# Kernel tuning notes

Measured on AMD Instinct MI355X. Metric: run time of the kernel, lower is better.

Reference implementation:

```python
import jax, jax.numpy as jnp
import numpy as np

N = 20000   # nodes
R = 8       # base out-degree (ring circulant), plus self-loop
K = 3       # hops: supports of A, A^2, A^3
IN_DIM = 128
HID = 64


def _edges(m):
    # support of A^m for circulant ring with self-loops: dst i receives from (i-t) mod N, t=0..m*R
    deg = m * R + 1
    dst = np.repeat(np.arange(N, dtype=np.int32), deg)
    src = (dst - np.tile(np.arange(deg, dtype=np.int32), N)) % N
    return jnp.asarray(src), jnp.asarray(dst)


def setup_inputs() -> dict:
    key = jax.random.key(0)
    ks = jax.random.split(key, 8)
    def xavier(k, shape):
        fan_out, fan_in = shape[0], shape[1]
        std = np.float32(np.sqrt(2.0) * np.sqrt(2.0 / (fan_in + fan_out)))  # gain('relu')
        return jax.random.normal(k, shape, jnp.float32) * std
    inp = {
        "h": jax.random.normal(ks[0], (N, IN_DIM), jnp.float32),
        "fc_enc": xavier(ks[1], (HID, IN_DIM)),
        "diff_enc": xavier(ks[2], (HID, IN_DIM)),
        "att_enc": xavier(ks[3], (HID, 1)),
        "fc_dec": xavier(ks[4], (IN_DIM, HID)),
        "diff_dec": xavier(ks[5], (IN_DIM, HID)),
        "att_dec": xavier(ks[6], (IN_DIM, 1)),
        "att_comb": xavier(ks[7], (HID, 1)),
    }
    for m in range(1, K + 1):
        s, d = _edges(m)
        inp[f"src{m}"] = s
        inp[f"dst{m}"] = d
    return inp


def _gdn_layer(src, dst, h, Wfc, Wdiff, att, use_elu):
    z = h @ Wfc.T                      # [N, out]
    hd = h @ Wdiff.T                   # [N, out]
    d = hd[src] - hd[dst]              # edge gather-diff [E, out]
    e = jax.nn.leaky_relu(d @ att)     # [E, 1], torch default slope 0.01
    # edge softmax over incoming edges of each dst node
    emax = jax.ops.segment_max(e, dst, num_segments=N)
    ex = jnp.exp(e - emax[dst])
    den = jax.ops.segment_sum(ex, dst, num_segments=N)
    a = ex / den[dst]                  # [E, 1]
    agg = jax.ops.segment_sum(a * d, dst, num_segments=N)  # scatter-sum
    out = z + agg
    return jax.nn.elu(out) if use_elu else out


def reference(h, fc_enc, diff_enc, att_enc, fc_dec, diff_dec, att_dec, att_comb,
              src1, dst1, src2, dst2, src3, dst3):
    hops = [(src1, dst1), (src2, dst2), (src3, dst3)]
    Zs = [_gdn_layer(s, d, h, fc_enc, diff_enc, att_enc, True) for s, d in hops]
    e = jnp.concatenate([Z @ att_comb for Z in Zs], axis=-1)   # [N, K]
    a = jax.nn.softmax(jax.nn.leaky_relu(e), axis=-1)          # [N, K]
    z = jnp.einsum('nk,nhk->nh', a, jnp.stack(Zs, axis=-1))    # hop-attention combine
    # decoder runs on the last hop's graph (A^K), as in the torch code
    x = _gdn_layer(src3, dst3, z, fc_dec, diff_dec, att_dec, False)
    return x
```

## Files before the change

### kernel.cpp

```cpp
#include <hip/hip_runtime.h>
#include <math.h>

#define NN 20000

typedef __attribute__((ext_vector_type(8))) short short8;
typedef __attribute__((ext_vector_type(4))) float floatx4;

__device__ __forceinline__ int wrapN(int r) {
    if (r < 0) r += NN;
    if (r >= NN) r -= NN;
    return r;
}
__device__ __forceinline__ unsigned f2bf(float f) {
    unsigned int u = __float_as_uint(f);
    u = (u + 0x7FFFu + ((u >> 16) & 1u)) >> 16;
    return u;
}

__global__ __launch_bounds__(256) void k0_prep(
    const float* __restrict__ fce, const float* __restrict__ dfe,
    const float* __restrict__ atte, const float* __restrict__ fcd,
    const float* __restrict__ dfd, const float* __restrict__ attd,
    unsigned short* __restrict__ Wenc, unsigned short* __restrict__ Wdec,
    float* __restrict__ uenc, float* __restrict__ vdec)
{
    const int idx = blockIdx.x * 256 + threadIdx.x;
    {
        int r = idx >> 7, k = idx & 127;
        float v = (r < 64) ? fce[r * 128 + k] : dfe[(r - 64) * 128 + k];
        Wenc[r * 128 + k] = (unsigned short)f2bf(v);
    }
    {
        int r = idx >> 6, k = idx & 63;
        float v = (r < 128) ? fcd[r * 64 + k] : dfd[(r - 128) * 64 + k];
        Wdec[r * 64 + k] = (unsigned short)f2bf(v);
    }
    if (blockIdx.x == 0 && threadIdx.x < 128) {
        int k = threadIdx.x; float s = 0.f;
        for (int j = 0; j < 64; j++) s = fmaf(atte[j], dfe[j * 128 + k], s);
        uenc[k] = s;
    }
    if (blockIdx.x == 1 && threadIdx.x < 64) {
        int k = threadIdx.x; float s = 0.f;
        for (int c = 0; c < 128; c++) s = fmaf(attd[c], dfd[c * 64 + k], s);
        vdec[k] = s;
    }
}

__global__ __launch_bounds__(256) void kA_enc(
    const float* __restrict__ h, const unsigned short* __restrict__ Wenc,
    const float* __restrict__ uenc, const float* __restrict__ attc,
    const float* __restrict__ vdec, unsigned short* __restrict__ zcb,
    float* __restrict__ gd)
{
    __shared__ __align__(16) float smem[3856];
    unsigned short* Hs = (unsigned short*)smem;
    float* hdw = smem;
    float* zw  = smem + 2720;
    float* gw  = smem + 3808;

    const int tid  = threadIdx.x;
    const int n0   = blockIdx.x * 16;
    const int lane = tid & 63;
    const int wv   = tid >> 6;
    const int m16  = lane & 15;
    const int quad = lane >> 4;

    for (int idx = tid; idx < 768; idx += 256) {
        int r = idx >> 4, c = (idx & 15) << 3;
        const float* hp = h + wrapN(n0 - 24 + r) * 128 + c;
        float4 a = *(const float4*)hp;
        float4 b = *(const float4*)(hp + 4);
        uint4 pk;
        pk.x = f2bf(a.x) | (f2bf(a.y) << 16);
        pk.y = f2bf(a.z) | (f2bf(a.w) << 16);
        pk.z = f2bf(b.x) | (f2bf(b.y) << 16);
        pk.w = f2bf(b.z) | (f2bf(b.w) << 16);
        *(uint4*)(Hs + r * 136 + c) = pk;
        float4 ua = *(const float4*)(uenc + c);
        float4 ub = *(const float4*)(uenc + c + 4);
        float p = a.x * ua.x + a.y * ua.y + a.z * ua.z + a.w * ua.w
                + b.x * ub.x + b.y * ub.y + b.z * ub.z + b.w * ub.w;
#pragma unroll
        for (int off = 1; off <= 8; off <<= 1) p += __shfl_xor(p, off, 64);
        if ((idx & 15) == 0) gw[r] = p;
    }
    __syncthreads();

    floatx4 acc[3][2];
#pragma unroll
    for (int a = 0; a < 3; a++)
#pragma unroll
        for (int b = 0; b < 2; b++) acc[a][b] = (floatx4){0.f, 0.f, 0.f, 0.f};

#pragma unroll
    for (int ks = 0; ks < 4; ks++) {
        const int kk = ks * 32 + quad * 8;
        const int jr0 = 32 * wv + m16;
        short8 B0 = *(const short8*)(Wenc + jr0 * 128 + kk);
        short8 B1 = *(const short8*)(Wenc + (jr0 + 16) * 128 + kk);
        short8 A[3];
#pragma unroll
        for (int mt = 0; mt < 3; mt++)
            A[mt] = *(short8*)(Hs + (mt * 16 + m16) * 136 + kk);
#pragma unroll
        for (int mt = 0; mt < 3; mt++) {
            acc[mt][0] = __builtin_amdgcn_mfma_f32_16x16x32_bf16(A[mt], B0, acc[mt][0], 0, 0, 0);
            acc[mt][1] = __builtin_amdgcn_mfma_f32_16x16x32_bf16(A[mt], B1, acc[mt][1], 0, 0, 0);
        }
    }
    __syncthreads();

#pragma unroll
    for (int mt = 0; mt < 3; mt++)
#pragma unroll
        for (int nt2 = 0; nt2 < 2; nt2++)
#pragma unroll
            for (int r = 0; r < 4; r++) {
                const int row = mt * 16 + quad * 4 + r;
                const int col = 32 * wv + nt2 * 16 + m16;
                const float val = acc[mt][nt2][r];
                if (col >= 64) { if (row < 40) hdw[row * 68 + (col - 64)] = val; }
                else if (row >= 24 && row < 40) zw[(row - 24) * 68 + col] = val;
            }
    __syncthreads();

    const int wvid = tid >> 6;
    const int half = (tid >> 5) & 1;
    const int l    = tid & 31;
    const float2 ac = *(const float2*)(attc + 2 * l);
    const float2 vd = *(const float2*)(vdec + 2 * l);

    for (int it = 0; it < 2; it++) {
        const int li   = 8 * it + 2 * wvid + half;
        const int node = n0 + li;
        const int loc  = 24 + li;

        const float g0 = gw[loc];
        const int t = l;
        float d = 0.f;
        if (t >= 1 && t < 25) {
            d = gw[loc - t] - g0;
            d = d > 0.f ? d : 0.01f * d;
        }
        float dm = (t < 25) ? d : -1e30f;
#pragma unroll
        for (int off = 16; off; off >>= 1) dm = fmaxf(dm, __shfl_xor(dm, off, 64));
        const float e = (t < 25) ? __expf(d - dm) : 0.f;
        float s1 = (t < 9) ? e : 0.f, s2 = (t < 17) ? e : 0.f, s3 = e;
#pragma unroll
        for (int off = 16; off; off >>= 1) {
            s1 += __shfl_xor(s1, off, 64);
            s2 += __shfl_xor(s2, off, 64);
            s3 += __shfl_xor(s3, off, 64);
        }
        const float rd0 = 1.f / s1, rd1 = 1.f / s2, rd2 = 1.f / s3;

        const float2 zi = *(const float2*)(zw + li * 68 + 2 * l);
        const float2 h0 = *(const float2*)(hdw + loc * 68 + 2 * l);

        float2 s = {0.f, 0.f};
        float2 Z[3]; float eh[3];
#pragma unroll
        for (int m = 0; m < 3; m++) {
            const int lo = (m == 0) ? 0 : (m == 1 ? 9 : 17);
            const int hi = (m == 0) ? 9 : (m == 1 ? 17 : 25);
#pragma unroll
            for (int t2 = lo; t2 < hi; t2++) {
                const float et = __shfl(e, (half << 5) + t2, 64);
                const float2 hv = *(const float2*)(hdw + (loc - t2) * 68 + 2 * l);
                s.x = fmaf(et, hv.x, s.x);
                s.y = fmaf(et, hv.y, s.y);
            }
            const float rden = (m == 0) ? rd0 : (m == 1 ? rd1 : rd2);
            float ox = zi.x + s.x * rden - h0.x;
            float oy = zi.y + s.y * rden - h0.y;
            Z[m].x = ox > 0.f ? ox : __expf(ox) - 1.f;
            Z[m].y = oy > 0.f ? oy : __expf(oy) - 1.f;
            float p = Z[m].x * ac.x + Z[m].y * ac.y;
#pragma unroll
            for (int off = 16; off; off >>= 1) p += __shfl_xor(p, off, 64);
            eh[m] = p;
        }
#pragma unroll
        for (int m = 0; m < 3; m++) eh[m] = eh[m] > 0.f ? eh[m] : 0.01f * eh[m];
        const float mx = fmaxf(eh[0], fmaxf(eh[1], eh[2]));
        const float w0 = __expf(eh[0] - mx), w1 = __expf(eh[1] - mx), w2 = __expf(eh[2] - mx);
        const float wd = 1.f / (w0 + w1 + w2);
        float2 o;
        o.x = (w0 * Z[0].x + w1 * Z[1].x + w2 * Z[2].x) * wd;
        o.y = (w0 * Z[0].y + w1 * Z[1].y + w2 * Z[2].y) * wd;
        *(unsigned int*)(zcb + node * 64 + 2 * l) =
            f2bf(o.x) | (f2bf(o.y) << 16);
        float q = o.x * vd.x + o.y * vd.y;
#pragma unroll
        for (int off = 16; off; off >>= 1) q += __shfl_xor(q, off, 64);
        if (l == 0) gd[node] = q;
    }
}

__global__ __launch_bounds__(256) void kB_dec(
    const unsigned short* __restrict__ zcb, const unsigned short* __restrict__ Wdec,
    const float* __restrict__ gd, float* __restrict__ out)
{
    __shared__ __align__(16) float smem[7928];
    unsigned short* Zs  = (unsigned short*)smem;
    unsigned short* hdB = (unsigned short*)smem;
    float* zdw = smem + 2304;
    float* h0w = smem + 4480;
    unsigned short* Eb = (unsigned short*)(smem + 6656);
    float* gw  = smem + 7808;
    float* dmw = smem + 7864;
    float* rdw = smem + 7896;

    const int tid  = threadIdx.x;
    const int tile = blockIdx.x >> 1;
    const int ch   = blockIdx.x & 1;
    const int n0   = tile * 32;
    const int lane = tid & 63;
    const int wv   = tid >> 6;
    const int m16  = lane & 15;
    const int quad = lane >> 4;

    if (tid < 56) gw[tid] = gd[wrapN(n0 - 24 + tid)];

    for (int idx = tid; idx < 512; idx += 256) {
        int r = idx >> 3, c = (idx & 7) << 3;
        *(short8*)(Zs + r * 72 + c) =
            *(const short8*)(zcb + wrapN(n0 - 24 + r) * 64 + c);
    }
    __syncthreads();

    floatx4 acc[4][2];
#pragma unroll
    for (int a = 0; a < 4; a++)
#pragma unroll
        for (int b = 0; b < 2; b++) acc[a][b] = (floatx4){0.f, 0.f, 0.f, 0.f};

#pragma unroll
    for (int ks = 0; ks < 2; ks++) {
        const int kk = ks * 32 + quad * 8;
        const int c0 = 32 * wv + m16;
        const int wr0 = (c0 < 64) ? (ch * 64 + c0) : (128 + ch * 64 + (c0 - 64));
        const int c1 = c0 + 16;
        const int wr1 = (c1 < 64) ? (ch * 64 + c1) : (128 + ch * 64 + (c1 - 64));
        short8 B0 = *(const short8*)(Wdec + wr0 * 64 + kk);
        short8 B1 = *(const short8*)(Wdec + wr1 * 64 + kk);
        short8 A[4];
#pragma unroll
        for (int mt = 0; mt < 4; mt++)
            A[mt] = *(short8*)(Zs + (mt * 16 + m16) * 72 + kk);
#pragma unroll
        for (int mt = 0; mt < 4; mt++) {
            acc[mt][0] = __builtin_amdgcn_mfma_f32_16x16x32_bf16(A[mt], B0, acc[mt][0], 0, 0, 0);
            acc[mt][1] = __builtin_amdgcn_mfma_f32_16x16x32_bf16(A[mt], B1, acc[mt][1], 0, 0, 0);
        }
    }
    __syncthreads();

#pragma unroll
    for (int mt = 0; mt < 4; mt++)
#pragma unroll
        for (int nt2 = 0; nt2 < 2; nt2++) {
            const int colL = 32 * wv + nt2 * 16 + m16;
            const int rowB = mt * 16 + quad * 4;
            if (colL >= 64) {
                const int f = colL - 64;
                if (rowB < 56) {
                    uint2 pk;
                    pk.x = f2bf(acc[mt][nt2][0]) | (f2bf(acc[mt][nt2][1]) << 16);
                    pk.y = f2bf(acc[mt][nt2][2]) | (f2bf(acc[mt][nt2][3]) << 16);
                    *(uint2*)(hdB + f * 72 + rowB) = pk;
                }
#pragma unroll
                for (int r = 0; r < 4; r++) {
                    const int row = rowB + r;
                    if (row >= 24 && row < 56) h0w[(row - 24) * 68 + f] = acc[mt][nt2][r];
                }
            } else {
#pragma unroll
                for (int r = 0; r < 4; r++) {
                    const int row = rowB + r;
                    if (row >= 24 && row < 56) zdw[(row - 24) * 68 + colL] = acc[mt][nt2][r];
                }
            }
        }
    for (int idx = tid; idx < 512; idx += 256) {
        int f = idx >> 3, kk = 56 + ((idx & 7) << 1);
        *(unsigned*)(hdB + f * 72 + kk) = 0;
    }

    {
        const int half = (tid >> 5) & 1;
        const int l    = tid & 31;
        for (int it = 0; it < 4; it++) {
            const int li  = 8 * it + 2 * wv + half;
            const int loc = 24 + li;
            const float g0 = gw[loc];
            const int t = l;
            float d = 0.f;
            if (t >= 1 && t < 25) {
                d = gw[loc - t] - g0;
                d = d > 0.f ? d : 0.01f * d;
            }
            float dm = (t < 25) ? d : -1e30f;
#pragma unroll
            for (int off = 16; off; off >>= 1) dm = fmaxf(dm, __shfl_xor(dm, off, 64));
            const float e = (t < 25) ? __expf(d - dm) : 0.f;
            float s3 = e;
#pragma unroll
            for (int off = 16; off; off >>= 1) s3 += __shfl_xor(s3, off, 64);
            if (l == 0) { dmw[li] = dm; rdw[li] = 1.f / s3; }
        }
    }
    __syncthreads();

    for (int idx = tid; idx < 1152; idx += 256) {
        const int n  = idx / 36;
        const int kk = (idx - n * 36) * 2;
        const float g0 = gw[n + 24];
        const float em = dmw[n], rd = rdw[n];
        unsigned pk = 0;
#pragma unroll
        for (int j = 0; j < 2; j++) {
            const int k = kk + j;
            const bool in = (k >= n) && (k <= n + 24);
            const int kc = in ? k : 0;
            float d = gw[kc] - g0;
            d = d > 0.f ? d : 0.01f * d;
            const float e = in ? __expf(d - em) * rd : 0.f;
            pk |= f2bf(e) << (16 * j);
        }
        *(unsigned*)(Eb + n * 72 + kk) = pk;
    }
    __syncthreads();

    floatx4 wacc[2];
    wacc[0] = (floatx4){0.f, 0.f, 0.f, 0.f};
    wacc[1] = (floatx4){0.f, 0.f, 0.f, 0.f};
#pragma unroll
    for (int ks = 0; ks < 2; ks++) {
        const int kk = ks * 32 + quad * 8;
        short8 Bf = *(short8*)(hdB + (wv * 16 + m16) * 72 + kk);
        short8 A0 = *(short8*)(Eb + m16 * 72 + kk);
        short8 A1 = *(short8*)(Eb + (16 + m16) * 72 + kk);
        wacc[0] = __builtin_amdgcn_mfma_f32_16x16x32_bf16(A0, Bf, wacc[0], 0, 0, 0);
        wacc[1] = __builtin_amdgcn_mfma_f32_16x16x32_bf16(A1, Bf, wacc[1], 0, 0, 0);
    }

#pragma unroll
    for (int mt2 = 0; mt2 < 2; mt2++)
#pragma unroll
        for (int r = 0; r < 4; r++) {
            const int n = mt2 * 16 + quad * 4 + r;
            const int f = wv * 16 + m16;
            const float o = zdw[n * 68 + f] + wacc[mt2][r] - h0w[n * 68 + f];
            out[(n0 + n) * 128 + ch * 64 + f] = o;
        }
}

extern "C" void kernel_launch(void* const* d_in, const int* in_sizes, int n_in,
                              void* d_out, int out_size, void* d_ws, size_t ws_size,
                              hipStream_t stream)
{
    const float* h        = (const float*)d_in[0];
    const float* fc_enc   = (const float*)d_in[1];
    const float* diff_enc = (const float*)d_in[2];
    const float* att_enc  = (const float*)d_in[3];
    const float* fc_dec   = (const float*)d_in[4];
    const float* diff_dec = (const float*)d_in[5];
    const float* att_dec  = (const float*)d_in[6];
    const float* att_comb = (const float*)d_in[7];

    float* out = (float*)d_out;
    float* ws  = (float*)d_ws;
    float*          uenc = ws;
    float*          vdec = ws + 128;
    float*          gd   = ws + 192;
    unsigned short* zcb  = (unsigned short*)(ws + 192 + NN);
    unsigned short* Wenc = zcb + NN * 64;
    unsigned short* Wdec = Wenc + 128 * 128;
    (void)ws_size; (void)in_sizes; (void)n_in; (void)out_size;

    hipLaunchKernelGGL(k0_prep, dim3(64), dim3(256), 0, stream,
                       fc_enc, diff_enc, att_enc, fc_dec, diff_dec, att_dec,
                       Wenc, Wdec, uenc, vdec);
    hipLaunchKernelGGL(kA_enc, dim3(NN / 16), dim3(256), 0, stream,
                       h, Wenc, uenc, att_comb, vdec, zcb, gd);
    hipLaunchKernelGGL(kB_dec, dim3(2 * (NN / 32)), dim3(256), 0, stream,
                       zcb, Wdec, gd, out);
}
```

Measured before the change: 121.6 us.

## Move encoder edge aggregation onto MFMA with banded softmax weight matrices

The encoder kernel now processes 32 nodes per block instead of 16, which reduces the redundant 24-row halo GEMM work per node. The per-node scalar shuffle-and-FMA aggregation over neighbor diffs is replaced by MFMA products. These multiply a bf16 hi/lo split of the hd tile against banded bf16 exp-weight matrices, one per hop, with the softmax normalisation done separately. The hop-attention reduction moves to shared memory across waves. This adds much more LDS use (about 52KB), extra syncs and bf16 rounding of the weights, in exchange for replacing many LDS loads and shuffles with matrix instructions.

```diff
diff --git a/kernel.cpp b/kernel.cpp
--- a/kernel.cpp
+++ b/kernel.cpp
@@ -15,6 +15,9 @@
     unsigned int u = __float_as_uint(f);
     u = (u + 0x7FFFu + ((u >> 16) & 1u)) >> 16;
     return u;
+}
+__device__ __forceinline__ float bfval(float f) {
+    return __uint_as_float(f2bf(f) << 16);
 }
 
 __global__ __launch_bounds__(256) void k0_prep(
@@ -47,26 +50,35 @@
     }
 }
 
-__global__ __launch_bounds__(256) void kA_enc(
+__global__ __launch_bounds__(256, 2) void kA_enc(
     const float* __restrict__ h, const unsigned short* __restrict__ Wenc,
     const float* __restrict__ uenc, const float* __restrict__ attc,
     const float* __restrict__ vdec, unsigned short* __restrict__ zcb,
     float* __restrict__ gd)
 {
-    __shared__ __align__(16) float smem[3856];
+    __shared__ __align__(16) float smem[13088];
+    float* zw  = smem;
+    float* h0w = smem + 2176;
+    unsigned short* hdB = (unsigned short*)(smem + 4352);
+    unsigned short* hdL = (unsigned short*)(smem + 6656);
+    unsigned short* Eb  = (unsigned short*)(smem + 8960);
+    float* gw  = smem + 12416;
+    float* dmw = smem + 12480;
+    float* rdw = smem + 12512;
+    float* ehp = smem + 12608;
+    float* ehw = smem + 12992;
     unsigned short* Hs = (unsigned short*)smem;
-    float* hdw = smem;
-    float* zw  = smem + 2720;
-    float* gw  = smem + 3808;
 
     const int tid  = threadIdx.x;
-    const int n0   = blockIdx.x * 16;
+    const int n0   = blockIdx.x * 32;
     const int lane = tid & 63;
     const int wv   = tid >> 6;
     const int m16  = lane & 15;
     const int quad = lane >> 4;
 
-    for (int idx = tid; idx < 768; idx += 256) {
+    for (int idx = tid; idx < 3456; idx += 256) ((unsigned*)Eb)[idx] = 0u;
+
+    for (int idx = tid; idx < 1024; idx += 256) {
         int r = idx >> 4, c = (idx & 15) << 3;
         const float* hp = h + wrapN(n0 - 24 + r) * 128 + c;
         float4 a = *(const float4*)hp;
@@ -87,9 +99,43 @@
     }
     __syncthreads();
 
-    floatx4 acc[3][2];
-#pragma unroll
-    for (int a = 0; a < 3; a++)
+    {
+        const int half = (tid >> 5) & 1;
+        const int l    = tid & 31;
+#pragma unroll
+        for (int it = 0; it < 4; it++) {
+            const int li  = 8 * it + 2 * wv + half;
+            const int loc = 24 + li;
+            const float g0 = gw[loc];
+            float d = 0.f;
+            if (l >= 1 && l < 25) {
+                d = gw[loc - l] - g0;
+                d = d > 0.f ? d : 0.01f * d;
+            }
+            float dm = (l < 25) ? d : -1e30f;
+#pragma unroll
+            for (int off = 16; off; off >>= 1) dm = fmaxf(dm, __shfl_xor(dm, off, 64));
+            const float e  = (l < 25) ? __expf(d - dm) : 0.f;
+            const float er = bfval(e);
+            float s1 = (l < 9) ? er : 0.f, s2 = (l < 17) ? er : 0.f, s3 = er;
+#pragma unroll
+            for (int off = 16; off; off >>= 1) {
+                s1 += __shfl_xor(s1, off, 64);
+                s2 += __shfl_xor(s2, off, 64);
+                s3 += __shfl_xor(s3, off, 64);
+            }
+            if (l == 0) {
+                dmw[li] = dm;
+                rdw[li]      = 1.f / s1;
+                rdw[32 + li] = 1.f / s2;
+                rdw[64 + li] = 1.f / s3;
+            }
+        }
+    }
+
+    floatx4 acc[4][2];
+#pragma unroll
+    for (int a = 0; a < 4; a++)
 #pragma unroll
         for (int b = 0; b < 2; b++) acc[a][b] = (floatx4){0.f, 0.f, 0.f, 0.f};
 
@@ -99,12 +145,12 @@
         const int jr0 = 32 * wv + m16;
         short8 B0 = *(const short8*)(Wenc + jr0 * 128 + kk);
         short8 B1 = *(const short8*)(Wenc + (jr0 + 16) * 128 + kk);
-        short8 A[3];
-#pragma unroll
-        for (int mt = 0; mt < 3; mt++)
+        short8 A[4];
+#pragma unroll
+        for (int mt = 0; mt < 4; mt++)
             A[mt] = *(short8*)(Hs + (mt * 16 + m16) * 136 + kk);
 #pragma unroll
-        for (int mt = 0; mt < 3; mt++) {
+        for (int mt = 0; mt < 4; mt++) {
             acc[mt][0] = __builtin_amdgcn_mfma_f32_16x16x32_bf16(A[mt], B0, acc[mt][0], 0, 0, 0);
             acc[mt][1] = __builtin_amdgcn_mfma_f32_16x16x32_bf16(A[mt], B1, acc[mt][1], 0, 0, 0);
         }
@@ -112,90 +158,158 @@
     __syncthreads();
 
 #pragma unroll
-    for (int mt = 0; mt < 3; mt++)
-#pragma unroll
-        for (int nt2 = 0; nt2 < 2; nt2++)
+    for (int mt = 0; mt < 4; mt++)
+#pragma unroll
+        for (int nt2 = 0; nt2 < 2; nt2++) {
+            const int colL = 32 * wv + nt2 * 16 + m16;
+            const int rowB = mt * 16 + quad * 4;
+            if (colL >= 64) {
+                const int f = colL - 64;
+                if (rowB < 56) {
+                    const unsigned b0 = f2bf(acc[mt][nt2][0]);
+                    const unsigned b1 = f2bf(acc[mt][nt2][1]);
+                    const unsigned b2 = f2bf(acc[mt][nt2][2]);
+                    const unsigned b3 = f2bf(acc[mt][nt2][3]);
+                    uint2 pk;
+                    pk.x = b0 | (b1 << 16);
+                    pk.y = b2 | (b3 << 16);
+                    *(uint2*)(hdB + f * 72 + rowB) = pk;
+                    uint2 pl;
+                    pl.x =  f2bf(acc[mt][nt2][0] - __uint_as_float(b0 << 16))
+                         | (f2bf(acc[mt][nt2][1] - __uint_as_float(b1 << 16)) << 16);
+                    pl.y =  f2bf(acc[mt][nt2][2] - __uint_as_float(b2 << 16))
+                         | (f2bf(acc[mt][nt2][3] - __uint_as_float(b3 << 16)) << 16);
+                    *(uint2*)(hdL + f * 72 + rowB) = pl;
+                }
+#pragma unroll
+                for (int r = 0; r < 4; r++) {
+                    const int row = rowB + r;
+                    if (row >= 24 && row < 56) h0w[(row - 24) * 68 + f] = acc[mt][nt2][r];
+                }
+            } else {
+#pragma unroll
+                for (int r = 0; r < 4; r++) {
+                    const int row = rowB + r;
+                    if (row >= 24 && row < 56) zw[(row - 24) * 68 + colL] = acc[mt][nt2][r];
+                }
+            }
+        }
+    for (int idx = tid; idx < 1024; idx += 256) {
+        const int j = idx & 511;
+        const int f = j >> 3, kk = 56 + ((j & 7) << 1);
+        unsigned short* p = (idx >> 9) ? hdL : hdB;
+        *(unsigned*)(p + f * 72 + kk) = 0u;
+    }
+
+    for (int idx = tid; idx < 800; idx += 256) {
+        const int n = idx / 25, t = idx - n * 25;
+        const int loc = n + 24;
+        float d = 0.f;
+        if (t >= 1) {
+            d = gw[loc - t] - gw[loc];
+            d = d > 0.f ? d : 0.01f * d;
+        }
+        const float e = __expf(d - dmw[n]);
+        const int m = (t < 9) ? 0 : ((t < 17) ? 1 : 2);
+        Eb[m * 2304 + n * 72 + (loc - t)] = (unsigned short)f2bf(e);
+    }
+    __syncthreads();
+
+    const int fbase = wv * 16 + quad * 4;
+    const float4 ac4 = *(const float4*)(attc + fbase);
+    short8 Af0 = *(short8*)(hdB + (wv * 16 + m16) * 72 + quad * 8);
+    short8 Af1 = *(short8*)(hdB + (wv * 16 + m16) * 72 + 32 + quad * 8);
+    short8 Al0 = *(short8*)(hdL + (wv * 16 + m16) * 72 + quad * 8);
+    short8 Al1 = *(short8*)(hdL + (wv * 16 + m16) * 72 + 32 + quad * 8);
+
+    floatx4 wacc[2];
+    wacc[0] = (floatx4){0.f, 0.f, 0.f, 0.f};
+    wacc[1] = (floatx4){0.f, 0.f, 0.f, 0.f};
+    float Zr[3][2][4];
+    float pm[3][2];
+#pragma unroll
+    for (int m = 0; m < 3; m++) { pm[m][0] = 0.f; pm[m][1] = 0.f; }
+
+#pragma unroll
+    for (int m = 0; m < 3; m++) {
+        const unsigned short* Em = Eb + m * 2304;
+        short8 E00 = *(const short8*)(Em + m16 * 72 + quad * 8);
+        short8 E01 = *(const short8*)(Em + m16 * 72 + 32 + quad * 8);
+        short8 E10 = *(const short8*)(Em + (16 + m16) * 72 + quad * 8);
+        short8 E11 = *(const short8*)(Em + (16 + m16) * 72 + 32 + quad * 8);
+        wacc[0] = __builtin_amdgcn_mfma_f32_16x16x32_bf16(Af0, E00, wacc[0], 0, 0, 0);
+        wacc[0] = __builtin_amdgcn_mfma_f32_16x16x32_bf16(Al0, E00, wacc[0], 0, 0, 0);
+        wacc[0] = __builtin_amdgcn_mfma_f32_16x16x32_bf16(Af1, E01, wacc[0], 0, 0, 0);
+        wacc[0] = __builtin_amdgcn_mfma_f32_16x16x32_bf16(Al1, E01, wacc[0], 0, 0, 0);
+        wacc[1] = __builtin_amdgcn_mfma_f32_16x16x32_bf16(Af0, E10, wacc[1], 0, 0, 0);
+        wacc[1] = __builtin_amdgcn_mfma_f32_16x16x32_bf16(Al0, E10, wacc[1], 0, 0, 0);
+        wacc[1] = __builtin_amdgcn_mfma_f32_16x16x32_bf16(Af1, E11, wacc[1], 0, 0, 0);
+        wacc[1] = __builtin_amdgcn_mfma_f32_16x16x32_bf16(Al1, E11, wacc[1], 0, 0, 0);
+#pragma unroll
+        for (int nt = 0; nt < 2; nt++) {
+            const int n = nt * 16 + m16;
+            const float rd = rdw[m * 32 + n];
+            const float4 zv = *(const float4*)(zw + n * 68 + fbase);
+            const float4 hv = *(const float4*)(h0w + n * 68 + fbase);
 #pragma unroll
             for (int r = 0; r < 4; r++) {
-                const int row = mt * 16 + quad * 4 + r;
-                const int col = 32 * wv + nt2 * 16 + m16;
-                const float val = acc[mt][nt2][r];
-                if (col >= 64) { if (row < 40) hdw[row * 68 + (col - 64)] = val; }
-                else if (row >= 24 && row < 40) zw[(row - 24) * 68 + col] = val;
-            }
-    __syncthreads();
-
-    const int wvid = tid >> 6;
-    const int half = (tid >> 5) & 1;
-    const int l    = tid & 31;
-    const float2 ac = *(const float2*)(attc + 2 * l);
-    const float2 vd = *(const float2*)(vdec + 2 * l);
-
-    for (int it = 0; it < 2; it++) {
-        const int li   = 8 * it + 2 * wvid + half;
-        const int node = n0 + li;
-        const int loc  = 24 + li;
-
-        const float g0 = gw[loc];
-        const int t = l;
-        float d = 0.f;
-        if (t >= 1 && t < 25) {
-            d = gw[loc - t] - g0;
-            d = d > 0.f ? d : 0.01f * d;
-        }
-        float dm = (t < 25) ? d : -1e30f;
-#pragma unroll
-        for (int off = 16; off; off >>= 1) dm = fmaxf(dm, __shfl_xor(dm, off, 64));
-        const float e = (t < 25) ? __expf(d - dm) : 0.f;
-        float s1 = (t < 9) ? e : 0.f, s2 = (t < 17) ? e : 0.f, s3 = e;
-#pragma unroll
-        for (int off = 16; off; off >>= 1) {
-            s1 += __shfl_xor(s1, off, 64);
-            s2 += __shfl_xor(s2, off, 64);
-            s3 += __shfl_xor(s3, off, 64);
-        }
-        const float rd0 = 1.f / s1, rd1 = 1.f / s2, rd2 = 1.f / s3;
-
-        const float2 zi = *(const float2*)(zw + li * 68 + 2 * l);
-        const float2 h0 = *(const float2*)(hdw + loc * 68 + 2 * l);
-
-        float2 s = {0.f, 0.f};
-        float2 Z[3]; float eh[3];
-#pragma unroll
-        for (int m = 0; m < 3; m++) {
-            const int lo = (m == 0) ? 0 : (m == 1 ? 9 : 17);
-            const int hi = (m == 0) ? 9 : (m == 1 ? 17 : 25);
-#pragma unroll
-            for (int t2 = lo; t2 < hi; t2++) {
-                const float et = __shfl(e, (half << 5) + t2, 64);
-                const float2 hv = *(const float2*)(hdw + (loc - t2) * 68 + 2 * l);
-                s.x = fmaf(et, hv.x, s.x);
-                s.y = fmaf(et, hv.y, s.y);
-            }
-            const float rden = (m == 0) ? rd0 : (m == 1 ? rd1 : rd2);
-            float ox = zi.x + s.x * rden - h0.x;
-            float oy = zi.y + s.y * rden - h0.y;
-            Z[m].x = ox > 0.f ? ox : __expf(ox) - 1.f;
-            Z[m].y = oy > 0.f ? oy : __expf(oy) - 1.f;
-            float p = Z[m].x * ac.x + Z[m].y * ac.y;
-#pragma unroll
-            for (int off = 16; off; off >>= 1) p += __shfl_xor(p, off, 64);
-            eh[m] = p;
-        }
-#pragma unroll
-        for (int m = 0; m < 3; m++) eh[m] = eh[m] > 0.f ? eh[m] : 0.01f * eh[m];
-        const float mx = fmaxf(eh[0], fmaxf(eh[1], eh[2]));
-        const float w0 = __expf(eh[0] - mx), w1 = __expf(eh[1] - mx), w2 = __expf(eh[2] - mx);
+                const float val = ((const float*)&zv)[r] + wacc[nt][r] * rd
+                                - ((const float*)&hv)[r];
+                const float z = val > 0.f ? val : __expf(val) - 1.f;
+                Zr[m][nt][r] = z;
+                pm[m][nt] = fmaf(z, ((const float*)&ac4)[r], pm[m][nt]);
+            }
+        }
+    }
+
+#pragma unroll
+    for (int m = 0; m < 3; m++)
+#pragma unroll
+        for (int nt = 0; nt < 2; nt++) {
+            float p = pm[m][nt];
+            p += __shfl_xor(p, 16, 64);
+            p += __shfl_xor(p, 32, 64);
+            pm[m][nt] = p;
+        }
+    if (quad == 0) {
+#pragma unroll
+        for (int nt = 0; nt < 2; nt++)
+#pragma unroll
+            for (int m = 0; m < 3; m++)
+                ehp[wv * 96 + (nt * 16 + m16) * 3 + m] = pm[m][nt];
+    }
+    __syncthreads();
+    if (tid < 96) {
+        const float s = ehp[tid] + ehp[96 + tid] + ehp[192 + tid] + ehp[288 + tid];
+        ehw[tid] = s > 0.f ? s : 0.01f * s;
+    }
+    __syncthreads();
+
+#pragma unroll
+    for (int nt = 0; nt < 2; nt++) {
+        const int n = nt * 16 + m16;
+        const float e0 = ehw[n * 3], e1 = ehw[n * 3 + 1], e2 = ehw[n * 3 + 2];
+        const float mx = fmaxf(e0, fmaxf(e1, e2));
+        const float w0 = __expf(e0 - mx), w1 = __expf(e1 - mx), w2 = __expf(e2 - mx);
         const float wd = 1.f / (w0 + w1 + w2);
-        float2 o;
-        o.x = (w0 * Z[0].x + w1 * Z[1].x + w2 * Z[2].x) * wd;
-        o.y = (w0 * Z[0].y + w1 * Z[1].y + w2 * Z[2].y) * wd;
-        *(unsigned int*)(zcb + node * 64 + 2 * l) =
-            f2bf(o.x) | (f2bf(o.y) << 16);
+        float4 o;
+        o.x = (w0 * Zr[0][nt][0] + w1 * Zr[1][nt][0] + w2 * Zr[2][nt][0]) * wd;
+        o.y = (w0 * Zr[0][nt][1] + w1 * Zr[1][nt][1] + w2 * Zr[2][nt][1]) * wd;
+        o.z = (w0 * Zr[0][nt][2] + w1 * Zr[1][nt][2] + w2 * Zr[2][nt][2]) * wd;
+        o.w = (w0 * Zr[0][nt][3] + w1 * Zr[1][nt][3] + w2 * Zr[2][nt][3]) * wd;
+        *(float4*)(zw + n * 68 + fbase) = o;
+    }
+    __syncthreads();
+
+    for (int idx = tid; idx < 1024; idx += 256) {
+        const int ln = idx >> 5, l = idx & 31;
+        const float2 o = *(const float2*)(zw + ln * 68 + 2 * l);
+        *(unsigned*)(zcb + (n0 + ln) * 64 + 2 * l) = f2bf(o.x) | (f2bf(o.y) << 16);
+        const float2 vd = *(const float2*)(vdec + 2 * l);
         float q = o.x * vd.x + o.y * vd.y;
 #pragma unroll
         for (int off = 16; off; off >>= 1) q += __shfl_xor(q, off, 64);
-        if (l == 0) gd[node] = q;
+        if (l == 0) gd[n0 + ln] = q;
     }
 }
 
@@ -385,7 +499,7 @@
     hipLaunchKernelGGL(k0_prep, dim3(64), dim3(256), 0, stream,
                        fc_enc, diff_enc, att_enc, fc_dec, diff_dec, att_dec,
                        Wenc, Wdec, uenc, vdec);
-    hipLaunchKernelGGL(kA_enc, dim3(NN / 16), dim3(256), 0, stream,
+    hipLaunchKernelGGL(kA_enc, dim3(NN / 32), dim3(256), 0, stream,
                        h, Wenc, uenc, att_comb, vdec, zcb, gd);
     hipLaunchKernelGGL(kB_dec, dim3(2 * (NN / 32)), dim3(256), 0, stream,
                        zcb, Wdec, gd, out);
```

Result: no change. 120.0 us (-1.3%).
